# Optimization experiments

Measured on AMD Instinct MI355X. Metric: run time of the kernel, lower is better.

The kernel has to match this reference:

```python
import jax, jax.numpy as jnp
import numpy as np

B, L, DIM, H, D, WS = 2, 2048, 1024, 16, 64, 256
SCALE = D ** -0.5


def _rope_tables(seq_len, dim, dtype):
    inv_freq = 1.0 / (10000.0 ** (jnp.arange(0, dim, 2, dtype=jnp.float32) / dim))
    t = jnp.arange(seq_len, dtype=jnp.float32)
    freqs = jnp.einsum('i,j->ij', t, inv_freq)          # [L, D/2]
    emb = jnp.concatenate([freqs, freqs], axis=-1)       # [L, D]
    return jnp.cos(emb).astype(dtype), jnp.sin(emb).astype(dtype)


def _rotate_half(x):
    x1, x2 = x[..., : x.shape[-1] // 2], x[..., x.shape[-1] // 2:]
    return jnp.concatenate([-x2, x1], axis=-1)


def _apply_rope(t, cos, sin):
    # t: [B, L, H, D]; cos/sin: [L, D] broadcast over batch and heads
    return t * cos[None, :, None, :] + _rotate_half(t) * sin[None, :, None, :]


def setup_inputs() -> dict:
    key = jax.random.key(0)
    k0, k1, k2 = jax.random.split(key, 3)
    x = jax.random.normal(k0, (B, L, DIM), dtype=jnp.float32)
    Wqkv = jax.random.normal(k1, (3 * H * D, DIM), dtype=jnp.float32) * 0.02
    bqkv = jnp.zeros((3 * H * D,), dtype=jnp.float32)
    Wproj = jax.random.normal(k2, (DIM, H * D), dtype=jnp.float32) * 0.02
    bproj = jnp.zeros((DIM,), dtype=jnp.float32)
    return {"x": x, "Wqkv": Wqkv, "bqkv": bqkv, "Wproj": Wproj, "bproj": bproj, "is_global": 1}


def _attention(x, Wqkv, bqkv, Wproj, bproj, is_global):
    b, l, _ = x.shape
    qkv = x @ Wqkv.T + bqkv                              # [B, L, 3*H*D]
    q, k, v = jnp.split(qkv, 3, axis=-1)
    q, k, v = (t.reshape(b, l, H, D) for t in (q, k, v))
    cos, sin = _rope_tables(l, D, x.dtype)
    q = _apply_rope(q, cos, sin)
    k = _apply_rope(k, cos, sin)
    if is_global:
        attn = jnp.einsum('bshd,bthd->bhst', q, k) * SCALE
        attn = jax.nn.softmax(attn, axis=-1)
        out = jnp.einsum('bhst,bthd->bshd', attn, v)     # [B, L, H, D]
    else:
        pad = (WS - l % WS) % WS
        if pad > 0:
            q, k, v = (jnp.pad(t, ((0, 0), (0, pad), (0, 0), (0, 0))) for t in (q, k, v))
        w = (l + pad) // WS
        q = q.reshape(b, w, WS, H, D)
        k = k.reshape(b, w, WS, H, D)
        v = v.reshape(b, w, WS, H, D)
        attn = jnp.einsum('bwshd,bwthd->bwhst', q, k) * SCALE
        attn = jax.nn.softmax(attn, axis=-1)
        out = jnp.einsum('bwhst,bwthd->bwshd', attn, v).reshape(b, w * WS, H, D)
        out = out[:, :l]
    return out.reshape(b, l, H * D) @ Wproj.T + bproj


def reference(x, Wqkv, bqkv, Wproj, bproj, is_global):
    return _attention(x, Wqkv, bqkv, Wproj, bproj, is_global)
```

## Files before the change

### kernel.cpp

```cpp
#include <hip/hip_runtime.h>
#include <math.h>

#define NB 2
#define NL 2048
#define NDIM 1024
#define NH 16
#define ND 64
#define NWS 256
#define NM (NB*NL)
#define QSCALE 0.18033688011112042f

typedef __attribute__((ext_vector_type(8))) short short8;
typedef __attribute__((ext_vector_type(4))) float f32x4;
typedef unsigned short ushort_t;
typedef unsigned int uint_t;

#define MFMA16(a,b,acc) __builtin_amdgcn_mfma_f32_16x16x32_bf16((a),(b),(acc),0,0,0)

static __device__ __forceinline__ ushort_t f2bf(float x){
    uint_t u = __float_as_uint(x);
    uint_t r = (u + 0x7fff + ((u >> 16) & 1)) >> 16;
    return (ushort_t)r;
}
static __device__ __forceinline__ float bf2f(ushort_t u){
    return __uint_as_float(((uint_t)u) << 16);
}
static __device__ __forceinline__ float fast_exp2(float x){
#if __has_builtin(__builtin_amdgcn_exp2f)
    return __builtin_amdgcn_exp2f(x);
#else
    return exp2f(x);
#endif
}

static __device__ __forceinline__ void async_load16(const void* g, void* l){
    __builtin_amdgcn_global_load_lds(
        (const __attribute__((address_space(1))) unsigned int*)g,
        (__attribute__((address_space(3))) unsigned int*)l, 16, 0, 0);
}

__launch_bounds__(256)
__global__ void split_all(const float* __restrict__ x,  ushort_t* __restrict__ xh,  ushort_t* __restrict__ xl,
                          const float* __restrict__ wq, ushort_t* __restrict__ wqh, ushort_t* __restrict__ wql,
                          const float* __restrict__ wp, ushort_t* __restrict__ wph, ushort_t* __restrict__ wpl)
{
    int i = blockIdx.x*256 + threadIdx.x;
    const float* in; ushort_t *oh, *ol;
    if (i < 1048576)      { in = x;  oh = xh;  ol = xl;  }
    else if (i < 1835008) { in = wq; oh = wqh; ol = wql; i -= 1048576; }
    else                  { in = wp; oh = wph; ol = wpl; i -= 1835008; }
    const int e = i*4;
    const float4 v = *(const float4*)(in + e);
    ushort_t h0=f2bf(v.x), h1=f2bf(v.y), h2=f2bf(v.z), h3=f2bf(v.w);
    ushort4 h4; h4.x=h0; h4.y=h1; h4.z=h2; h4.w=h3;
    ushort4 l4;
    l4.x=f2bf(v.x - bf2f(h0)); l4.y=f2bf(v.y - bf2f(h1));
    l4.z=f2bf(v.z - bf2f(h2)); l4.w=f2bf(v.w - bf2f(h3));
    *(ushort4*)(oh + e) = h4;
    *(ushort4*)(ol + e) = l4;
}

__launch_bounds__(256)
__global__ void rope_tab(float* __restrict__ tc, float* __restrict__ ts)
{
    const int idx = blockIdx.x*256 + threadIdx.x;
    const int j = idx >> 11, l = idx & (NL-1);
    const float invf = 1.0f / powf(10000.0f, (float)j * (1.0f/32.0f));
    float s, c;
    sincosf((float)l * invf, &s, &c);
    tc[idx] = c; ts[idx] = s;
}

template<int MODE>
__launch_bounds__(256, 2)
__global__ void gemm_hl(const ushort_t* __restrict__ Ah, const ushort_t* __restrict__ Al,
                        const ushort_t* __restrict__ Bh, const ushort_t* __restrict__ Bl,
                        const float* __restrict__ bias,
                        float* __restrict__ Cout,
                        ushort_t* __restrict__ oQh, ushort_t* __restrict__ oKh,
                        ushort_t* __restrict__ oVth,
                        const float* __restrict__ tcos, const float* __restrict__ tsin)
{
    __shared__ __align__(16) char smem[74752];
    ushort_t* sA_h = (ushort_t*)smem;
    ushort_t* sA_l = (ushort_t*)(smem + 8192);
    ushort_t* sB_h = (ushort_t*)(smem + 16384);
    ushort_t* sB_l = (ushort_t*)(smem + 20480);
    ushort_t* sBounce = (ushort_t*)smem;
    const int ebuf = 12288;
    const int bbuf = 24576;
    const int NTT  = (MODE==0) ? 4 : 2;
    const int WN   = (MODE==0) ? 64 : 32;

    const int tid  = threadIdx.x;
    const int wv   = tid >> 6, lane = tid & 63;
    const int quad = lane >> 4, l16 = lane & 15;
    const int m0 = blockIdx.y << 7, n0 = blockIdx.x * ((MODE==0) ? 128 : 64);
    const int wr = wv >> 1, wc = wv & 1;

    const int rl = lane >> 2;
    const int cp = lane & 3;
    const int cg = cp ^ ((rl >> 1) & 3);
    const ushort_t* pAh = Ah + (size_t)(m0 + 32*wv + rl)*NDIM + cg*8;
    const ushort_t* pAl = Al + (size_t)(m0 + 32*wv + rl)*NDIM + cg*8;
    const ushort_t* pBh;
    const ushort_t* pBl;
    if (MODE == 0) { pBh = Bh + (size_t)(n0 + 32*wv + rl)*NDIM + cg*8; pBl = pBh; }
    else { pBh = Bh + (size_t)(n0 + 16*wv + rl)*NDIM + cg*8;
           pBl = Bl + (size_t)(n0 + 16*wv + rl)*NDIM + cg*8; }
    char* dA  = smem + wv*2048;
    char* dB0 = smem + 16384 + ((MODE==0) ? wv*2048 : wv*1024);
    char* dB1 = smem + 20480 + wv*1024;

    f32x4 acc[4][NTT];
    #pragma unroll
    for (int i=0;i<4;++i)
        #pragma unroll
        for (int j=0;j<NTT;++j) acc[i][j] = (f32x4){0.f,0.f,0.f,0.f};

    const int swz = (l16 >> 1) & 3;
    const int ac_off = (wr*64 + l16)*32 + ((quad ^ swz) << 3);
    const int bc_off = (wc*WN + l16)*32 + ((quad ^ swz) << 3);

#define GSTAGE(SLOT, KOFF) do { \
        const int so_ = (SLOT)*bbuf; \
        async_load16(pAh + (KOFF),           dA + so_); \
        async_load16(pAh + 16*NDIM + (KOFF), dA + so_ + 1024); \
        async_load16(pAl + (KOFF),           dA + so_ + 8192); \
        async_load16(pAl + 16*NDIM + (KOFF), dA + so_ + 9216); \
        if (MODE == 0) { \
            async_load16(pBh + (KOFF),           dB0 + so_); \
            async_load16(pBh + 16*NDIM + (KOFF), dB0 + so_ + 1024); \
        } else { \
            async_load16(pBh + (KOFF), dB0 + so_); \
            async_load16(pBl + (KOFF), dB1 + so_); \
        } \
    } while(0)

#define GCOMP(SLOT) do { \
        const int eo_ = (SLOT)*ebuf; \
        short8 ah[4], al[4], bh[NTT], bl[NTT]; \
        _Pragma("unroll") \
        for (int t=0;t<4;++t){ \
            ah[t] = *(const short8*)&sA_h[eo_ + t*512 + ac_off]; \
            al[t] = *(const short8*)&sA_l[eo_ + t*512 + ac_off]; \
        } \
        _Pragma("unroll") \
        for (int t=0;t<NTT;++t){ \
            bh[t] = *(const short8*)&sB_h[eo_ + t*512 + bc_off]; \
            if (MODE == 1) bl[t] = *(const short8*)&sB_l[eo_ + t*512 + bc_off]; \
        } \
        _Pragma("unroll") \
        for (int mt=0;mt<4;++mt) \
            _Pragma("unroll") \
            for (int nt=0;nt<NTT;++nt){ \
                f32x4 a_ = acc[mt][nt]; \
                a_ = MFMA16(ah[mt], bh[nt], a_); \
                a_ = MFMA16(al[mt], bh[nt], a_); \
                if (MODE == 1) a_ = MFMA16(ah[mt], bl[nt], a_); \
                acc[mt][nt] = a_; \
            } \
    } while(0)

#define GPHASE(SLOT, K0, VN) do { \
        asm volatile("s_waitcnt vmcnt(" #VN ")" ::: "memory"); \
        __builtin_amdgcn_sched_barrier(0); \
        __builtin_amdgcn_s_barrier(); \
        __builtin_amdgcn_sched_barrier(0); \
        GCOMP(SLOT); \
        asm volatile("s_waitcnt lgkmcnt(0)" ::: "memory"); \
        __builtin_amdgcn_sched_barrier(0); \
        __builtin_amdgcn_s_barrier(); \
        __builtin_amdgcn_sched_barrier(0); \
        if ((K0) + 96 < NDIM) GSTAGE(SLOT, (K0) + 96); \
    } while(0)

    GSTAGE(0, 0); GSTAGE(1, 32); GSTAGE(2, 64);
    for (int k0 = 0; k0 < 960; k0 += 96) {
        GPHASE(0, k0,      12);
        GPHASE(1, k0 + 32, 12);
        GPHASE(2, k0 + 64, 12);
    }
    GPHASE(0, 960, 0);
    GPHASE(1, 992, 0);
#undef GSTAGE
#undef GCOMP
#undef GPHASE

    if (MODE == 1) {
        const int colb = n0 + wc*32;
        float bq[2];
        #pragma unroll
        for (int nt=0;nt<2;++nt) bq[nt] = bias[colb + nt*16 + l16];
        #pragma unroll
        for (int mt=0;mt<4;++mt)
            #pragma unroll
            for (int r=0;r<4;++r){
                const int m = m0 + wr*64 + mt*16 + quad*4 + r;
                float* orow = Cout + (size_t)m*NDIM + colb;
                #pragma unroll
                for (int nt=0;nt<2;++nt)
                    orow[nt*16 + l16] = acc[mt][nt][r] + bq[nt];
            }
    } else {
        const int colb = n0 + wc*64;
        const int sel  = colb >> 10;
        const int head = (colb & 1023) >> 6;
        float bq[4];
        #pragma unroll
        for (int nt=0;nt<4;++nt) bq[nt] = bias[colb + nt*16 + l16];

        if (sel == 2) {
            __syncthreads();
            const int bb = m0 >> 11;
            const int Lb = (m0 & (NL-1)) + wr*64;
            ushort_t* sT = sBounce + wv*(64*72);
            const size_t gb = ((size_t)(bb*NH + head)*ND)*NL + Lb;
            const int drow = lane >> 3, dcol = lane & 7;
            #pragma unroll
            for (int mt=0;mt<4;++mt)
                #pragma unroll
                for (int nt=0;nt<4;++nt)
                    #pragma unroll
                    for (int r=0;r<4;++r)
                        sT[(nt*16+l16)*72 + mt*16 + quad*4 + r] = f2bf(acc[mt][nt][r] + bq[nt]);
            #pragma unroll
            for (int dd=0; dd<8; ++dd){
                const int d = dd*8 + drow;
                const uint4 v = *(const uint4*)&sT[d*72 + dcol*8];
                *(uint4*)(oVth + gb + (size_t)d*NL + dcol*8) = v;
            }
        } else {
            ushort_t* dh = sel ? oKh : oQh;
            const float qs = sel ? 1.0f : QSCALE;
            #pragma unroll
            for (int mt=0;mt<4;++mt)
                #pragma unroll
                for (int r=0;r<4;++r){
                    const int m = m0 + wr*64 + mt*16 + quad*4 + r;
                    const int bb = m >> 11, l = m & (NL-1);
                    const size_t ro = ((size_t)((bb*NH + head)*NL + l)) << 6;
                    #pragma unroll
                    for (int ntp=0;ntp<2;++ntp){
                        const int j = ntp*16 + l16;
                        const float c = tcos[j*NL + l];
                        const float s = tsin[j*NL + l];
                        const float x1 = acc[mt][ntp  ][r] + bq[ntp];
                        const float x2 = acc[mt][ntp+2][r] + bq[ntp+2];
                        const int d1 = ntp*16 + l16;
                        dh[ro + d1]      = f2bf((x1*c - x2*s) * qs);
                        dh[ro + d1 + 32] = f2bf((x2*c + x1*s) * qs);
                    }
                }
        }
    }
}

__launch_bounds__(256, 4)
__global__ void attn_mfma(const ushort_t* __restrict__ Qh,
                          const ushort_t* __restrict__ Kh,
                          const ushort_t* __restrict__ Vth,
                          ushort_t* __restrict__ AOh, ushort_t* __restrict__ AOl,
                          const int* __restrict__ isg)
{
    __shared__ __align__(16) char smem[40960];

    const int tid  = threadIdx.x;
    const int wv   = tid >> 6, lane = tid & 63;
    const int quad = lane >> 4, l16 = lane & 15;
    const int bh = blockIdx.x & 31, qt = blockIdx.x >> 5;
    const int q0w = qt*64 + wv*16;

    short8 bq0, bq1;
    {
        const size_t rb = (((size_t)bh*NL + q0w) << 6) + (size_t)(l16 << 6) + quad*8;
        bq0 = *(const short8*)(Qh + rb);
        bq1 = *(const short8*)(Qh + rb + 32);
    }
    short8 ones;
    #pragma unroll
    for (int j=0;j<8;++j) ones[j] = (short)0x3F80;

    f32x4 o[4];
    #pragma unroll
    for (int dnt=0; dnt<4; ++dnt) o[dnt] = (f32x4){0.f,0.f,0.f,0.f};
    f32x4 lsacc = (f32x4){0.f,0.f,0.f,0.f};

    const int gflag = isg[0];
    int klo, khi;
    if (gflag) { klo = 0; khi = NL; }
    else       { klo = (qt >> 2)*NWS; khi = klo + NWS; }

    const int swz4 = (l16 & 7) << 4;
    const int KC0 = l16*128 + (( quad*16      ) ^ swz4);
    const int KC1 = l16*128 + (( quad*16 + 64 ) ^ swz4);
    const int sPb = 32768 + wv*2048;
    int PW[4];
    #pragma unroll
    for (int knt=0; knt<4; ++knt)
        PW[knt] = sPb + l16*128 + ((knt*32 + quad*8) ^ swz4);
    const int PR0 = sPb + KC0;
    const int PR1 = sPb + KC1;

    const int r8  = lane >> 3;
    const int c8s = (lane & 7) ^ r8;
    const ushort_t* Kp = Kh + (((size_t)bh*NL) << 6)
                       + (size_t)(klo + wv*16 + r8)*64 + c8s*8;
    const ushort_t* Vp = Vth + (size_t)bh*ND*NL
                       + (size_t)(wv*16 + r8)*NL + klo + c8s*8;
    const int kdst = wv*2048;
    const int vdst = 16384 + wv*2048;

#define STAGE(BUF) do { \
        async_load16(Kp,          smem + (BUF)*8192 + kdst); \
        async_load16(Kp + 512,    smem + (BUF)*8192 + kdst + 1024); \
        async_load16(Vp,          smem + (BUF)*8192 + vdst); \
        async_load16(Vp + 8*NL,   smem + (BUF)*8192 + vdst + 1024); \
        Kp += 64*64; Vp += 64; } while (0)

#define TILE(BUF) do { \
        const char* kb_ = smem + (BUF)*8192; \
        const char* vb_ = smem + 16384 + (BUF)*8192; \
        f32x4 s_[4]; \
        _Pragma("unroll") \
        for (int knt=0; knt<4; ++knt) { \
            const short8 a0 = *(const short8*)(kb_ + knt*2048 + KC0); \
            const short8 a1 = *(const short8*)(kb_ + knt*2048 + KC1); \
            f32x4 t = (f32x4){0.f,0.f,0.f,0.f}; \
            t = MFMA16(a0, bq0, t); \
            t = MFMA16(a1, bq1, t); \
            s_[knt] = t; \
        } \
        _Pragma("unroll") \
        for (int knt=0; knt<4; ++knt) { \
            const uint_t u0 = __float_as_uint(fast_exp2(s_[knt][0])); \
            const uint_t u1 = __float_as_uint(fast_exp2(s_[knt][1])); \
            const uint_t u2 = __float_as_uint(fast_exp2(s_[knt][2])); \
            const uint_t u3 = __float_as_uint(fast_exp2(s_[knt][3])); \
            uint2 pk_; \
            pk_.x = __builtin_amdgcn_perm(u1, u0, 0x07060302u); \
            pk_.y = __builtin_amdgcn_perm(u3, u2, 0x07060302u); \
            *(uint2*)(smem + PW[knt]) = pk_; \
        } \
        const short8 fp0 = *(const short8*)(smem + PR0); \
        const short8 fp1 = *(const short8*)(smem + PR1); \
        lsacc = MFMA16(fp0, ones, lsacc); \
        lsacc = MFMA16(fp1, ones, lsacc); \
        _Pragma("unroll") \
        for (int dnt=0; dnt<4; ++dnt) { \
            const short8 v0 = *(const short8*)(vb_ + dnt*2048 + KC0); \
            const short8 v1 = *(const short8*)(vb_ + dnt*2048 + KC1); \
            f32x4 t = o[dnt]; \
            t = MFMA16(fp0, v0, t); \
            t = MFMA16(fp1, v1, t); \
            o[dnt] = t; \
        } } while (0)

    STAGE(0);
    for (int kt = klo; kt < khi; kt += 128) {
        __syncthreads();
        if (kt + 64 < khi) STAGE(1);
        TILE(0);
        __syncthreads();
        if (kt + 128 < khi) STAGE(0);
        TILE(1);
    }
#undef STAGE
#undef TILE

    const int bb = bh >> 4, hh = bh & 15;
    #pragma unroll
    for (int r=0; r<4; ++r) {
        const float inv = 1.0f / lsacc[r];
        const int row = q0w + quad*4 + r;
        const size_t ob = (((size_t)(bb*NL + row)) << 10) + (hh << 6);
        #pragma unroll
        for (int dnt=0; dnt<4; ++dnt) {
            const float val = o[dnt][r] * inv;
            const ushort_t h = f2bf(val);
            AOh[ob + dnt*16 + l16] = h;
            AOl[ob + dnt*16 + l16] = f2bf(val - bf2f(h));
        }
    }
}

extern "C" void kernel_launch(void* const* d_in, const int* in_sizes, int n_in,
                              void* d_out, int out_size, void* d_ws, size_t ws_size,
                              hipStream_t stream)
{
    const float* x     = (const float*)d_in[0];
    const float* Wqkv  = (const float*)d_in[1];
    const float* bqkv  = (const float*)d_in[2];
    const float* Wproj = (const float*)d_in[3];
    const float* bproj = (const float*)d_in[4];
    const int*   isg   = (const int*)d_in[5];
    float* out = (float*)d_out;
    char* base = (char*)d_ws;

    const size_t MB = 1024*1024;
    ushort_t* Qh  = (ushort_t*)(base);
    ushort_t* Kh  = (ushort_t*)(base + 16*MB);
    ushort_t* Vth = (ushort_t*)(base + 32*MB);
    ushort_t* xh  = (ushort_t*)(base + 48*MB);
    ushort_t* xl  = (ushort_t*)(base + 56*MB);
    ushort_t* AOh = xh;
    ushort_t* AOl = xl;
    ushort_t* Wqh = (ushort_t*)(base + 64*MB);
    ushort_t* Wql = (ushort_t*)(base + 64*MB + 6291456);
    ushort_t* Wph = (ushort_t*)(base + 76*MB);
    ushort_t* Wpl = (ushort_t*)(base + 76*MB + 2097152);
    float*    tcs = (float*)(base + 80*MB);
    float*    tsn = (float*)(base + 80*MB + 262144);

    split_all<<<8192, 256, 0, stream>>>(x, xh, xl, Wqkv, Wqh, Wql, Wproj, Wph, Wpl);
    rope_tab<<<256, 256, 0, stream>>>(tcs, tsn);

    gemm_hl<0><<<dim3(3*NDIM/128, NM/128), 256, 0, stream>>>(
        xh, xl, Wqh, Wql, bqkv, nullptr,
        Qh, Kh, Vth, tcs, tsn);

    attn_mfma<<<NB*NH*(NL/64), 256, 0, stream>>>(
        Qh, Kh, Vth, AOh, AOl, isg);

    gemm_hl<1><<<dim3(NDIM/64, NM/128), 256, 0, stream>>>(
        AOh, AOl, Wph, Wpl, bproj, out,
        nullptr, nullptr, nullptr, nullptr, nullptr);
}
```

Measured before the change: 226.5 us.

## Split QKV GEMM into dedicated kernel with warp-specialized loads and double buffering

Replaces the templated GEMM with two kernels. The QKV GEMM now uses two LDS buffers instead of three, with 50 KB of shared memory, and is launched with launch_bounds(256,3) to allow higher occupancy. Global-to-LDS loads are split by wave: one wave loads A-high, one loads A-low, two load B. It also switches to __syncthreads-based double buffering. The aim is better occupancy and latency hiding, but the load work per wave is unbalanced and the pipeline is shallower.

```diff
diff --git a/kernel.cpp b/kernel.cpp
--- a/kernel.cpp
+++ b/kernel.cpp
@@ -71,31 +71,157 @@
     tc[idx] = c; ts[idx] = s;
 }
 
-template<int MODE>
+__launch_bounds__(256, 3)
+__global__ void gemm_qkv(const ushort_t* __restrict__ Ah, const ushort_t* __restrict__ Al,
+                         const ushort_t* __restrict__ Bh,
+                         const float* __restrict__ bias,
+                         ushort_t* __restrict__ oQh, ushort_t* __restrict__ oKh,
+                         ushort_t* __restrict__ oVth,
+                         const float* __restrict__ tcos, const float* __restrict__ tsin)
+{
+    __shared__ __align__(16) char smem[50176];
+    ushort_t* sA_h = (ushort_t*)smem;
+    ushort_t* sA_l = (ushort_t*)(smem + 8192);
+    ushort_t* sB_h = (ushort_t*)(smem + 16384);
+    ushort_t* sBounce = (ushort_t*)smem;
+    const int ebuf = 12288;
+    const int bbuf = 24576;
+
+    const int tid  = threadIdx.x;
+    const int wv   = tid >> 6, lane = tid & 63;
+    const int quad = lane >> 4, l16 = lane & 15;
+    const int m0 = blockIdx.y << 7, n0 = blockIdx.x << 7;
+    const int wr = wv >> 1, wc = wv & 1;
+
+    const ushort_t* gsrc;
+    ushort_t* lds_base;
+    int rowb, npass;
+    if (wv == 0)      { gsrc = Ah; lds_base = sA_h; rowb = m0; npass = 8; }
+    else if (wv == 1) { gsrc = Al; lds_base = sA_l; rowb = m0; npass = 8; }
+    else { gsrc = Bh; lds_base = sB_h + (wv-2)*64*32; rowb = n0 + (wv-2)*64; npass = 4; }
+    const int rl = lane >> 2;
+    const int cp = lane & 3;
+    const int cg = cp ^ ((rl >> 1) & 3);
+    const ushort_t* gptr = gsrc + (size_t)(rowb + rl)*NDIM + cg*8;
+
+    f32x4 acc[4][4];
+    #pragma unroll
+    for (int i=0;i<4;++i)
+        #pragma unroll
+        for (int j=0;j<4;++j) acc[i][j] = (f32x4){0.f,0.f,0.f,0.f};
+
+    const int swz = (l16 >> 1) & 3;
+    const int ac_off = (wr*64 + l16)*32 + ((quad ^ swz) << 3);
+    const int bc_off = (wc*64 + l16)*32 + ((quad ^ swz) << 3);
+
+#define QSTAGE(BUF, KOFF) do { \
+        const ushort_t* gp_ = gptr + (KOFF); \
+        for (int p=0; p<npass; ++p) \
+            async_load16(gp_ + (size_t)p*16*NDIM, (char*)lds_base + (BUF)*bbuf + p*1024); \
+    } while(0)
+
+#define QCOMP(BUF) do { \
+        const int eo_ = (BUF)*ebuf; \
+        short8 ah[4], al[4], bh[4]; \
+        _Pragma("unroll") \
+        for (int t=0;t<4;++t){ \
+            ah[t] = *(const short8*)&sA_h[eo_ + t*512 + ac_off]; \
+            al[t] = *(const short8*)&sA_l[eo_ + t*512 + ac_off]; \
+            bh[t] = *(const short8*)&sB_h[eo_ + t*512 + bc_off]; \
+        } \
+        _Pragma("unroll") \
+        for (int mt=0;mt<4;++mt) \
+            _Pragma("unroll") \
+            for (int nt=0;nt<4;++nt){ \
+                f32x4 a_ = acc[mt][nt]; \
+                a_ = MFMA16(ah[mt], bh[nt], a_); \
+                a_ = MFMA16(al[mt], bh[nt], a_); \
+                acc[mt][nt] = a_; \
+            } \
+    } while(0)
+
+    QSTAGE(0, 0);
+    for (int k0 = 0; k0 < NDIM; k0 += 64) {
+        __syncthreads();
+        QSTAGE(1, k0 + 32);
+        QCOMP(0);
+        __syncthreads();
+        if (k0 + 64 < NDIM) QSTAGE(0, k0 + 64);
+        QCOMP(1);
+    }
+#undef QSTAGE
+#undef QCOMP
+
+    const int colb = n0 + wc*64;
+    const int sel  = colb >> 10;
+    const int head = (colb & 1023) >> 6;
+    float bq[4];
+    #pragma unroll
+    for (int nt=0;nt<4;++nt) bq[nt] = bias[colb + nt*16 + l16];
+
+    if (sel == 2) {
+        __syncthreads();
+        const int bb = m0 >> 11;
+        const int Lb = (m0 & (NL-1)) + wr*64;
+        ushort_t* sT = sBounce + wv*(64*72);
+        const size_t gb = ((size_t)(bb*NH + head)*ND)*NL + Lb;
+        const int drow = lane >> 3, dcol = lane & 7;
+        #pragma unroll
+        for (int mt=0;mt<4;++mt)
+            #pragma unroll
+            for (int nt=0;nt<4;++nt)
+                #pragma unroll
+                for (int r=0;r<4;++r)
+                    sT[(nt*16+l16)*72 + mt*16 + quad*4 + r] = f2bf(acc[mt][nt][r] + bq[nt]);
+        #pragma unroll
+        for (int dd=0; dd<8; ++dd){
+            const int d = dd*8 + drow;
+            const uint4 v = *(const uint4*)&sT[d*72 + dcol*8];
+            *(uint4*)(oVth + gb + (size_t)d*NL + dcol*8) = v;
+        }
+    } else {
+        ushort_t* dh = sel ? oKh : oQh;
+        const float qs = sel ? 1.0f : QSCALE;
+        #pragma unroll
+        for (int mt=0;mt<4;++mt)
+            #pragma unroll
+            for (int r=0;r<4;++r){
+                const int m = m0 + wr*64 + mt*16 + quad*4 + r;
+                const int bb = m >> 11, l = m & (NL-1);
+                const size_t ro = ((size_t)((bb*NH + head)*NL + l)) << 6;
+                #pragma unroll
+                for (int ntp=0;ntp<2;++ntp){
+                    const int j = ntp*16 + l16;
+                    const float c = tcos[j*NL + l];
+                    const float s = tsin[j*NL + l];
+                    const float x1 = acc[mt][ntp  ][r] + bq[ntp];
+                    const float x2 = acc[mt][ntp+2][r] + bq[ntp+2];
+                    const int d1 = ntp*16 + l16;
+                    dh[ro + d1]      = f2bf((x1*c - x2*s) * qs);
+                    dh[ro + d1 + 32] = f2bf((x2*c + x1*s) * qs);
+                }
+            }
+    }
+}
+
 __launch_bounds__(256, 2)
-__global__ void gemm_hl(const ushort_t* __restrict__ Ah, const ushort_t* __restrict__ Al,
-                        const ushort_t* __restrict__ Bh, const ushort_t* __restrict__ Bl,
-                        const float* __restrict__ bias,
-                        float* __restrict__ Cout,
-                        ushort_t* __restrict__ oQh, ushort_t* __restrict__ oKh,
-                        ushort_t* __restrict__ oVth,
-                        const float* __restrict__ tcos, const float* __restrict__ tsin)
+__global__ void gemm_proj(const ushort_t* __restrict__ Ah, const ushort_t* __restrict__ Al,
+                          const ushort_t* __restrict__ Bh, const ushort_t* __restrict__ Bl,
+                          const float* __restrict__ bias,
+                          float* __restrict__ Cout)
 {
     __shared__ __align__(16) char smem[74752];
     ushort_t* sA_h = (ushort_t*)smem;
     ushort_t* sA_l = (ushort_t*)(smem + 8192);
     ushort_t* sB_h = (ushort_t*)(smem + 16384);
     ushort_t* sB_l = (ushort_t*)(smem + 20480);
-    ushort_t* sBounce = (ushort_t*)smem;
     const int ebuf = 12288;
     const int bbuf = 24576;
-    const int NTT  = (MODE==0) ? 4 : 2;
-    const int WN   = (MODE==0) ? 64 : 32;
 
     const int tid  = threadIdx.x;
     const int wv   = tid >> 6, lane = tid & 63;
     const int quad = lane >> 4, l16 = lane & 15;
-    const int m0 = blockIdx.y << 7, n0 = blockIdx.x * ((MODE==0) ? 128 : 64);
+    const int m0 = blockIdx.y << 7, n0 = blockIdx.x << 6;
     const int wr = wv >> 1, wc = wv & 1;
 
     const int rl = lane >> 2;
@@ -103,157 +229,96 @@
     const int cg = cp ^ ((rl >> 1) & 3);
     const ushort_t* pAh = Ah + (size_t)(m0 + 32*wv + rl)*NDIM + cg*8;
     const ushort_t* pAl = Al + (size_t)(m0 + 32*wv + rl)*NDIM + cg*8;
-    const ushort_t* pBh;
-    const ushort_t* pBl;
-    if (MODE == 0) { pBh = Bh + (size_t)(n0 + 32*wv + rl)*NDIM + cg*8; pBl = pBh; }
-    else { pBh = Bh + (size_t)(n0 + 16*wv + rl)*NDIM + cg*8;
-           pBl = Bl + (size_t)(n0 + 16*wv + rl)*NDIM + cg*8; }
+    const ushort_t* pBh = Bh + (size_t)(n0 + 16*wv + rl)*NDIM + cg*8;
+    const ushort_t* pBl = Bl + (size_t)(n0 + 16*wv + rl)*NDIM + cg*8;
     char* dA  = smem + wv*2048;
-    char* dB0 = smem + 16384 + ((MODE==0) ? wv*2048 : wv*1024);
+    char* dB0 = smem + 16384 + wv*1024;
     char* dB1 = smem + 20480 + wv*1024;
 
-    f32x4 acc[4][NTT];
+    f32x4 acc[4][2];
     #pragma unroll
     for (int i=0;i<4;++i)
         #pragma unroll
-        for (int j=0;j<NTT;++j) acc[i][j] = (f32x4){0.f,0.f,0.f,0.f};
+        for (int j=0;j<2;++j) acc[i][j] = (f32x4){0.f,0.f,0.f,0.f};
 
     const int swz = (l16 >> 1) & 3;
     const int ac_off = (wr*64 + l16)*32 + ((quad ^ swz) << 3);
-    const int bc_off = (wc*WN + l16)*32 + ((quad ^ swz) << 3);
-
-#define GSTAGE(SLOT, KOFF) do { \
+    const int bc_off = (wc*32 + l16)*32 + ((quad ^ swz) << 3);
+
+#define PSTAGE(SLOT, KOFF) do { \
         const int so_ = (SLOT)*bbuf; \
         async_load16(pAh + (KOFF),           dA + so_); \
         async_load16(pAh + 16*NDIM + (KOFF), dA + so_ + 1024); \
         async_load16(pAl + (KOFF),           dA + so_ + 8192); \
         async_load16(pAl + 16*NDIM + (KOFF), dA + so_ + 9216); \
-        if (MODE == 0) { \
-            async_load16(pBh + (KOFF),           dB0 + so_); \
-            async_load16(pBh + 16*NDIM + (KOFF), dB0 + so_ + 1024); \
-        } else { \
-            async_load16(pBh + (KOFF), dB0 + so_); \
-            async_load16(pBl + (KOFF), dB1 + so_); \
-        } \
+        async_load16(pBh + (KOFF), dB0 + so_); \
+        async_load16(pBl + (KOFF), dB1 + so_); \
     } while(0)
 
-#define GCOMP(SLOT) do { \
+#define PCOMP(SLOT) do { \
         const int eo_ = (SLOT)*ebuf; \
-        short8 ah[4], al[4], bh[NTT], bl[NTT]; \
+        short8 ah[4], al[4], bh[2], bl[2]; \
         _Pragma("unroll") \
         for (int t=0;t<4;++t){ \
             ah[t] = *(const short8*)&sA_h[eo_ + t*512 + ac_off]; \
             al[t] = *(const short8*)&sA_l[eo_ + t*512 + ac_off]; \
         } \
         _Pragma("unroll") \
-        for (int t=0;t<NTT;++t){ \
+        for (int t=0;t<2;++t){ \
             bh[t] = *(const short8*)&sB_h[eo_ + t*512 + bc_off]; \
-            if (MODE == 1) bl[t] = *(const short8*)&sB_l[eo_ + t*512 + bc_off]; \
+            bl[t] = *(const short8*)&sB_l[eo_ + t*512 + bc_off]; \
         } \
         _Pragma("unroll") \
         for (int mt=0;mt<4;++mt) \
             _Pragma("unroll") \
-            for (int nt=0;nt<NTT;++nt){ \
+            for (int nt=0;nt<2;++nt){ \
                 f32x4 a_ = acc[mt][nt]; \
                 a_ = MFMA16(ah[mt], bh[nt], a_); \
                 a_ = MFMA16(al[mt], bh[nt], a_); \
-                if (MODE == 1) a_ = MFMA16(ah[mt], bl[nt], a_); \
+                a_ = MFMA16(ah[mt], bl[nt], a_); \
                 acc[mt][nt] = a_; \
             } \
     } while(0)
 
-#define GPHASE(SLOT, K0, VN) do { \
+#define PPHASE(SLOT, K0, VN) do { \
         asm volatile("s_waitcnt vmcnt(" #VN ")" ::: "memory"); \
         __builtin_amdgcn_sched_barrier(0); \
         __builtin_amdgcn_s_barrier(); \
         __builtin_amdgcn_sched_barrier(0); \
-        GCOMP(SLOT); \
+        PCOMP(SLOT); \
         asm volatile("s_waitcnt lgkmcnt(0)" ::: "memory"); \
         __builtin_amdgcn_sched_barrier(0); \
         __builtin_amdgcn_s_barrier(); \
         __builtin_amdgcn_sched_barrier(0); \
-        if ((K0) + 96 < NDIM) GSTAGE(SLOT, (K0) + 96); \
+        if ((K0) + 96 < NDIM) PSTAGE(SLOT, (K0) + 96); \
     } while(0)
 
-    GSTAGE(0, 0); GSTAGE(1, 32); GSTAGE(2, 64);
+    PSTAGE(0, 0); PSTAGE(1, 32); PSTAGE(2, 64);
     for (int k0 = 0; k0 < 960; k0 += 96) {
-        GPHASE(0, k0,      12);
-        GPHASE(1, k0 + 32, 12);
-        GPHASE(2, k0 + 64, 12);
-    }
-    GPHASE(0, 960, 0);
-    GPHASE(1, 992, 0);
-#undef GSTAGE
-#undef GCOMP
-#undef GPHASE
-
-    if (MODE == 1) {
-        const int colb = n0 + wc*32;
-        float bq[2];
-        #pragma unroll
-        for (int nt=0;nt<2;++nt) bq[nt] = bias[colb + nt*16 + l16];
-        #pragma unroll
-        for (int mt=0;mt<4;++mt)
+        PPHASE(0, k0,      12);
+        PPHASE(1, k0 + 32, 12);
+        PPHASE(2, k0 + 64, 12);
+    }
+    PPHASE(0, 960, 0);
+    PPHASE(1, 992, 0);
+#undef PSTAGE
+#undef PCOMP
+#undef PPHASE
+
+    const int colb = n0 + wc*32;
+    float bq[2];
+    #pragma unroll
+    for (int nt=0;nt<2;++nt) bq[nt] = bias[colb + nt*16 + l16];
+    #pragma unroll
+    for (int mt=0;mt<4;++mt)
+        #pragma unroll
+        for (int r=0;r<4;++r){
+            const int m = m0 + wr*64 + mt*16 + quad*4 + r;
+            float* orow = Cout + (size_t)m*NDIM + colb;
             #pragma unroll
-            for (int r=0;r<4;++r){
-                const int m = m0 + wr*64 + mt*16 + quad*4 + r;
-                float* orow = Cout + (size_t)m*NDIM + colb;
-                #pragma unroll
-                for (int nt=0;nt<2;++nt)
-                    orow[nt*16 + l16] = acc[mt][nt][r] + bq[nt];
-            }
-    } else {
-        const int colb = n0 + wc*64;
-        const int sel  = colb >> 10;
-        const int head = (colb & 1023) >> 6;
-        float bq[4];
-        #pragma unroll
-        for (int nt=0;nt<4;++nt) bq[nt] = bias[colb + nt*16 + l16];
-
-        if (sel == 2) {
-            __syncthreads();
-            const int bb = m0 >> 11;
-            const int Lb = (m0 & (NL-1)) + wr*64;
-            ushort_t* sT = sBounce + wv*(64*72);
-            const size_t gb = ((size_t)(bb*NH + head)*ND)*NL + Lb;
-            const int drow = lane >> 3, dcol = lane & 7;
-            #pragma unroll
-            for (int mt=0;mt<4;++mt)
-                #pragma unroll
-                for (int nt=0;nt<4;++nt)
-                    #pragma unroll
-                    for (int r=0;r<4;++r)
-                        sT[(nt*16+l16)*72 + mt*16 + quad*4 + r] = f2bf(acc[mt][nt][r] + bq[nt]);
-            #pragma unroll
-            for (int dd=0; dd<8; ++dd){
-                const int d = dd*8 + drow;
-                const uint4 v = *(const uint4*)&sT[d*72 + dcol*8];
-                *(uint4*)(oVth + gb + (size_t)d*NL + dcol*8) = v;
-            }
-        } else {
-            ushort_t* dh = sel ? oKh : oQh;
-            const float qs = sel ? 1.0f : QSCALE;
-            #pragma unroll
-            for (int mt=0;mt<4;++mt)
-                #pragma unroll
-                for (int r=0;r<4;++r){
-                    const int m = m0 + wr*64 + mt*16 + quad*4 + r;
-                    const int bb = m >> 11, l = m & (NL-1);
-                    const size_t ro = ((size_t)((bb*NH + head)*NL + l)) << 6;
-                    #pragma unroll
-                    for (int ntp=0;ntp<2;++ntp){
-                        const int j = ntp*16 + l16;
-                        const float c = tcos[j*NL + l];
-                        const float s = tsin[j*NL + l];
-                        const float x1 = acc[mt][ntp  ][r] + bq[ntp];
-                        const float x2 = acc[mt][ntp+2][r] + bq[ntp+2];
-                        const int d1 = ntp*16 + l16;
-                        dh[ro + d1]      = f2bf((x1*c - x2*s) * qs);
-                        dh[ro + d1 + 32] = f2bf((x2*c + x1*s) * qs);
-                    }
-                }
+            for (int nt=0;nt<2;++nt)
+                orow[nt*16 + l16] = acc[mt][nt][r] + bq[nt];
         }
-    }
 }
 
 __launch_bounds__(256, 4)
@@ -415,14 +480,12 @@
     split_all<<<8192, 256, 0, stream>>>(x, xh, xl, Wqkv, Wqh, Wql, Wproj, Wph, Wpl);
     rope_tab<<<256, 256, 0, stream>>>(tcs, tsn);
 
-    gemm_hl<0><<<dim3(3*NDIM/128, NM/128), 256, 0, stream>>>(
-        xh, xl, Wqh, Wql, bqkv, nullptr,
-        Qh, Kh, Vth, tcs, tsn);
+    gemm_qkv<<<dim3(3*NDIM/128, NM/128), 256, 0, stream>>>(
+        xh, xl, Wqh, bqkv, Qh, Kh, Vth, tcs, tsn);
 
     attn_mfma<<<NB*NH*(NL/64), 256, 0, stream>>>(
         Qh, Kh, Vth, AOh, AOl, isg);
 
-    gemm_hl<1><<<dim3(NDIM/64, NM/128), 256, 0, stream>>>(
-        AOh, AOl, Wph, Wpl, bproj, out,
-        nullptr, nullptr, nullptr, nullptr, nullptr);
-}
+    gemm_proj<<<dim3(NDIM/64, NM/128), 256, 0, stream>>>(
+        AOh, AOl, Wph, Wpl, bproj, out);
+}
```

Result: no change. 223.3 us (-1.4%).
